# Kernel tuning notes

Measured on AMD Instinct MI355X. Metric: run time of the kernel, lower is better.

The kernel has to match this reference:

```python
import jax, jax.numpy as jnp
import numpy as np

N_NODES = 50000
N_EDGES = 400000
NUM_FEAT = 11
HID = 64
LAT = 64
HEADS = 3
MAX_NODES = 29
NUM_GRAPHS = 2048
NEG_SLOPE = 0.2


def _w(key, shape):
    return (jax.random.normal(key, shape) * 0.05).astype(jnp.float32)


def setup_inputs() -> dict:
    key = jax.random.key(0)
    ks = jax.random.split(key, 32)
    x = jax.random.normal(ks[0], (N_NODES, NUM_FEAT), dtype=jnp.float32)
    edge_index = jax.random.randint(ks[1], (2, N_EDGES), 0, N_NODES, dtype=jnp.int64)
    batch = jnp.sort(jax.random.randint(ks[2], (N_NODES,), 0, NUM_GRAPHS, dtype=jnp.int64))
    d = {"x": x, "edge_index": edge_index, "batch": batch}
    # GATv2 layer params: lin_l, lin_r ([in, heads*out]), att [heads,out], bias [out]
    dims = [(NUM_FEAT, HID), (HID, 2 * HID), (2 * HID, 4 * HID)]
    k = 3
    for i, (cin, cout) in enumerate(dims, start=1):
        d[f"Wl{i}"] = _w(ks[k], (cin, HEADS * cout)); k += 1
        d[f"bl{i}"] = jnp.zeros((HEADS * cout,), jnp.float32)
        d[f"Wr{i}"] = _w(ks[k], (cin, HEADS * cout)); k += 1
        d[f"br{i}"] = jnp.zeros((HEADS * cout,), jnp.float32)
        d[f"att{i}"] = _w(ks[k], (HEADS, cout)); k += 1
        d[f"b{i}"] = jnp.zeros((cout,), jnp.float32)
    d["Wmu"] = _w(ks[k], (4 * HID, LAT)); k += 1
    d["bmu"] = jnp.zeros((LAT,), jnp.float32)
    d["Wlv"] = _w(ks[k], (4 * HID, LAT)); k += 1
    d["blv"] = jnp.zeros((LAT,), jnp.float32)
    out_dim = MAX_NODES * NUM_FEAT + MAX_NODES * MAX_NODES
    d["Wd1"] = _w(ks[k], (LAT, 4 * HID)); k += 1
    d["bd1"] = jnp.zeros((4 * HID,), jnp.float32)
    d["Wd2"] = _w(ks[k], (4 * HID, 8 * HID)); k += 1
    d["bd2"] = jnp.zeros((8 * HID,), jnp.float32)
    d["Wd3"] = _w(ks[k], (8 * HID, out_dim)); k += 1
    d["bd3"] = jnp.zeros((out_dim,), jnp.float32)
    return d


def _gatv2(x, src, dst, Wl, bl, Wr, br, att, bias):
    # GATv2Conv, heads=HEADS, concat=False (mean over heads), self-loops already in src/dst
    N = x.shape[0]
    H, C = att.shape
    xl = (x @ Wl + bl).reshape(N, H, C)  # source transform
    xr = (x @ Wr + br).reshape(N, H, C)  # target transform
    e = jax.nn.leaky_relu(xl[src] + xr[dst], NEG_SLOPE)  # [E,H,C]
    logits = jnp.einsum('ehc,hc->eh', e, att)            # [E,H]
    mx = jax.ops.segment_max(logits, dst, num_segments=N)
    a = jnp.exp(logits - mx[dst])
    denom = jax.ops.segment_sum(a, dst, num_segments=N)
    alpha = a / (denom[dst] + 1e-16)
    out = jax.ops.segment_sum(alpha[:, :, None] * xl[src], dst, num_segments=N)  # [N,H,C]
    return out.mean(axis=1) + bias


def reference(x, edge_index, batch,
              Wl1, bl1, Wr1, br1, att1, b1,
              Wl2, bl2, Wr2, br2, att2, b2,
              Wl3, bl3, Wr3, br3, att3, b3,
              Wmu, bmu, Wlv, blv,
              Wd1, bd1, Wd2, bd2, Wd3, bd3):
    N = x.shape[0]
    loops = jnp.arange(N, dtype=edge_index.dtype)
    src = jnp.concatenate([edge_index[0], loops])
    dst = jnp.concatenate([edge_index[1], loops])
    h = jax.nn.relu(_gatv2(x, src, dst, Wl1, bl1, Wr1, br1, att1, b1))
    h = jax.nn.relu(_gatv2(h, src, dst, Wl2, bl2, Wr2, br2, att2, b2))
    h = jax.nn.relu(_gatv2(h, src, dst, Wl3, bl3, Wr3, br3, att3, b3))
    g = jax.ops.segment_sum(h, batch, num_segments=NUM_GRAPHS)  # global_add_pool
    mu = g @ Wmu + bmu
    logvar = g @ Wlv + blv
    z = mu  # deterministic decode of the posterior mean (no forward() given)
    o = jax.nn.relu(z @ Wd1 + bd1)
    o = jax.nn.relu(o @ Wd2 + bd2)
    o = o @ Wd3 + bd3
    nsplit = MAX_NODES * NUM_FEAT
    x_rec = o[:, :nsplit].reshape(-1, MAX_NODES, NUM_FEAT)
    adj = o[:, nsplit:].reshape(-1, MAX_NODES, MAX_NODES)
    adj_rec = (adj + jnp.swapaxes(adj, 1, 2)) / 2
    return (x_rec, adj_rec, mu, logvar)
```

## Files before the change

### kernel.cpp

```cpp
#include <hip/hip_runtime.h>
#include <hip/hip_bf16.h>

typedef __hip_bfloat16 bf16;
typedef unsigned short ushortT;
typedef ushortT u16x2 __attribute__((ext_vector_type(2)));
typedef ushortT u16x4 __attribute__((ext_vector_type(4)));
typedef ushortT u16x8 __attribute__((ext_vector_type(8)));
typedef __bf16   bf16x8 __attribute__((ext_vector_type(8)));
typedef float    f32x4  __attribute__((ext_vector_type(4)));

#define N_NODES    50000
#define E_EDGES    400000
#define E_TOT      450000
#define NUM_GRAPHS 2048
#define SCAN_CHUNK 1024
#define N_CHUNKS   ((N_NODES + SCAN_CHUNK - 1) / SCAN_CHUNK)

__device__ __forceinline__ float fromb(ushortT u) {
    unsigned int i = ((unsigned int)u) << 16;
    return __builtin_bit_cast(float, i);
}
__device__ __forceinline__ ushortT tob(float v) {
    bf16 h = __float2bfloat16(v);
    return __builtin_bit_cast(ushortT, h);
}

template <int VEC> struct RawV;
template <> struct RawV<1> { using T = ushortT; };
template <> struct RawV<2> { using T = u16x2; };
template <> struct RawV<4> { using T = u16x4; };

__device__ __forceinline__ void cvtv(ushortT r, float* f) { f[0] = fromb(r); }
__device__ __forceinline__ void cvtv(u16x2 r, float* f)   { f[0] = fromb(r.x); f[1] = fromb(r.y); }
__device__ __forceinline__ void cvtv(u16x4 r, float* f)   { f[0] = fromb(r.x); f[1] = fromb(r.y);
                                                            f[2] = fromb(r.z); f[3] = fromb(r.w); }

__global__ void diag_kernel(float* out, float v) { if (threadIdx.x == 0) out[0] = v; }

__global__ void hist_kernel(const int* __restrict__ ei, int* __restrict__ counts) {
    int e = blockIdx.x * 256 + threadIdx.x;
    if (e >= E_TOT) return;
    int d = (e < E_EDGES) ? ei[E_EDGES + e] : (e - E_EDGES);
    atomicAdd(&counts[d], 1);
}

__global__ __launch_bounds__(256) void scan_sums(const int* __restrict__ counts,
                                                 int* __restrict__ chunk_sums) {
    __shared__ int red[4];
    int base = blockIdx.x * SCAN_CHUNK;
    int t = threadIdx.x;
    int s = 0;
    #pragma unroll
    for (int i = 0; i < 4; i++) {
        int idx = base + t + i * 256;
        if (idx < N_NODES) s += counts[idx];
    }
    #pragma unroll
    for (int o = 32; o > 0; o >>= 1) s += __shfl_xor(s, o);
    if ((t & 63) == 0) red[t >> 6] = s;
    __syncthreads();
    if (t == 0) chunk_sums[blockIdx.x] = red[0] + red[1] + red[2] + red[3];
}

__global__ __launch_bounds__(64) void scan_chunks(const int* __restrict__ chunk_sums,
                                                  int* __restrict__ chunk_base) {
    int t = threadIdx.x;
    int v = (t < N_CHUNKS) ? chunk_sums[t] : 0;
    int orig = v;
    #pragma unroll
    for (int o = 1; o < 64; o <<= 1) {
        int u = __shfl_up(v, o);
        if (t >= o) v += u;
    }
    if (t < N_CHUNKS) chunk_base[t] = v - orig;
}

__global__ __launch_bounds__(256) void scan_write(const int* __restrict__ counts,
                                                  const int* __restrict__ chunk_base,
                                                  int* __restrict__ offsets) {
    __shared__ int wsum[4];
    int chunk = blockIdx.x;
    int base = chunk * SCAN_CHUNK;
    int t = threadIdx.x;
    int lane = t & 63, w = t >> 6;

    int c[4];
    int e0 = base + t * 4;
    #pragma unroll
    for (int k = 0; k < 4; k++) {
        int idx = e0 + k;
        c[k] = (idx < N_NODES) ? counts[idx] : 0;
    }
    int local = c[0] + c[1] + c[2] + c[3];

    int v = local;
    #pragma unroll
    for (int o = 1; o < 64; o <<= 1) {
        int u = __shfl_up(v, o);
        if (lane >= o) v += u;
    }
    if (lane == 63) wsum[w] = v;
    __syncthreads();
    int wbase = 0;
    for (int i = 0; i < w; i++) wbase += wsum[i];

    int run = chunk_base[chunk] + wbase + (v - local);
    #pragma unroll
    for (int k = 0; k < 4; k++) {
        int idx = e0 + k;
        if (idx < N_NODES) offsets[idx] = run;
        run += c[k];
    }
    if (chunk == 0 && t == 0) offsets[N_NODES] = E_TOT;
}

__global__ void copy_kernel(const int* __restrict__ src, int* __restrict__ dst, int n) {
    int i = blockIdx.x * 256 + threadIdx.x;
    if (i < n) dst[i] = src[i];
}

__global__ void scatter_kernel(const int* __restrict__ ei, int* __restrict__ cursor,
                               int* __restrict__ srcs) {
    int e = blockIdx.x * 256 + threadIdx.x;
    if (e >= E_TOT) return;
    int s, d;
    if (e < E_EDGES) { s = ei[e]; d = ei[E_EDGES + e]; }
    else             { s = d = e - E_EDGES; }
    int pos = atomicAdd(&cursor[d], 1);
    srcs[pos] = s;
}

__global__ void repack_kernel(const float* __restrict__ W, ushortT* __restrict__ Bp,
                              int K, int N) {
    int idx = blockIdx.x * 256 + threadIdx.x;
    if (idx >= K * N) return;
    int k = idx / N, n = idx % N;
    Bp[((size_t)(k >> 3) * N + n) * 8 + (k & 7)] = tob(W[idx]);
}

__global__ void repack_split(const float* __restrict__ W, ushortT* __restrict__ Bh,
                             ushortT* __restrict__ Bl, int K, int N, int Npad) {
    int idx = blockIdx.x * 256 + threadIdx.x;
    if (idx >= K * Npad) return;
    int k = idx / Npad, n = idx % Npad;
    float v = (n < N) ? W[(size_t)k * N + n] : 0.f;
    ushortT h = tob(v);
    float r = v - fromb(h);
    size_t o = ((size_t)(k >> 3) * Npad + n) * 8 + (k & 7);
    Bh[o] = h;
    Bl[o] = tob(r);
}

__global__ __launch_bounds__(192) void l1_transform(const float* __restrict__ x,
                                                    const float* __restrict__ Wl,
                                                    const float* __restrict__ bl,
                                                    const float* __restrict__ Wr,
                                                    const float* __restrict__ br,
                                                    ushortT* __restrict__ XL,
                                                    ushortT* __restrict__ XR, int M) {
    __shared__ float xs[64][11];
    const int tid = threadIdx.x;
    const int bm  = blockIdx.x * 64;
    const int rows = (M - bm < 64) ? (M - bm) : 64;

    float wl[11], wr[11];
    #pragma unroll
    for (int k = 0; k < 11; k++) {
        wl[k] = Wl[k * 192 + tid];
        wr[k] = Wr[k * 192 + tid];
    }
    float blc = bl[tid], brc = br[tid];

    for (int i = tid; i < rows * 11; i += 192)
        xs[i / 11][i % 11] = x[(size_t)bm * 11 + i];
    __syncthreads();

    for (int r = 0; r < rows; r++) {
        float al = blc, ar = brc;
        #pragma unroll
        for (int k = 0; k < 11; k++) {
            float xv = xs[r][k];
            al += xv * wl[k];
            ar += xv * wr[k];
        }
        size_t o = (size_t)(bm + r) * 192 + tid;
        XL[o] = tob(al);
        XR[o] = tob(ar);
    }
}

template <bool RELU>
__global__ __launch_bounds__(256) void gemm_dec(const float* __restrict__ A,
                                                const float* __restrict__ B,
                                                const float* __restrict__ bias,
                                                float* __restrict__ C,
                                                int M, int N, int K,
                                                int lda, int ldb, int ldc) {
    __shared__ float As[32][33];
    __shared__ float Bs[32][65];
    int tid = threadIdx.x;
    int tm = tid >> 4, tn = tid & 15;
    int bm = blockIdx.y * 32, bn = blockIdx.x * 64;
    float acc[2][4] = {};
    for (int k0 = 0; k0 < K; k0 += 32) {
        #pragma unroll
        for (int i = 0; i < 4; i++) {
            int e = tid + i * 256;
            int r = e >> 5, k = e & 31;
            int row = bm + r, kk = k0 + k;
            float v = 0.f;
            if (row < M && kk < K) v = A[(size_t)row * lda + kk];
            As[k][r] = v;
        }
        #pragma unroll
        for (int i = 0; i < 8; i++) {
            int e = tid + i * 256;
            int k = e >> 6, n = e & 63;
            int kk = k0 + k, col = bn + n;
            float v = 0.f;
            if (kk < K && col < N) v = B[(size_t)kk * ldb + col];
            Bs[k][n] = v;
        }
        __syncthreads();
        #pragma unroll
        for (int k = 0; k < 32; k++) {
            float a0 = As[k][tm * 2 + 0], a1 = As[k][tm * 2 + 1];
            float b0 = Bs[k][tn * 4 + 0], b1 = Bs[k][tn * 4 + 1];
            float b2 = Bs[k][tn * 4 + 2], b3 = Bs[k][tn * 4 + 3];
            acc[0][0] += a0 * b0; acc[0][1] += a0 * b1; acc[0][2] += a0 * b2; acc[0][3] += a0 * b3;
            acc[1][0] += a1 * b0; acc[1][1] += a1 * b1; acc[1][2] += a1 * b2; acc[1][3] += a1 * b3;
        }
        __syncthreads();
    }
    #pragma unroll
    for (int i = 0; i < 2; i++) {
        int row = bm + tm * 2 + i;
        if (row >= M) continue;
        #pragma unroll
        for (int j = 0; j < 4; j++) {
            int col = bn + tn * 4 + j;
            if (col >= N) continue;
            float v = acc[i][j] + bias[col];
            if (RELU) v = fmaxf(v, 0.f);
            C[(size_t)row * ldc + col] = v;
        }
    }
}

template <bool RELU>
__global__ __launch_bounds__(256) void mfma_dec(const float* __restrict__ A,
                                                const ushortT* __restrict__ Bh,
                                                const ushortT* __restrict__ Bl,
                                                const float* __restrict__ bias,
                                                float* __restrict__ C,
                                                int M, int N, int K, int Npad,
                                                int lda, int ldc) {
    __shared__ ushortT Ah[4 * 128 * 8];
    __shared__ ushortT Al[4 * 128 * 8];
    const int tid = threadIdx.x;
    const int bm = blockIdx.y * 128;
    const int bn = blockIdx.x * 128;
    const int lane = tid & 63;
    const int l15 = lane & 15, lg = lane >> 4;
    const int wid = tid >> 6;
    const int wm = wid >> 1, wn = wid & 1;

    f32x4 acc[4][4] = {};

    for (int k0 = 0; k0 < K; k0 += 32) {
        __syncthreads();
        #pragma unroll
        for (int it = 0; it < 2; it++) {
            int c = tid + it * 256;
            int row = c >> 2, kg = c & 3;
            const float* ap = A + (size_t)(bm + row) * lda + k0 + kg * 8;
            u16x8 hv, lv;
            #pragma unroll
            for (int i = 0; i < 8; i++) {
                float v = ap[i];
                ushortT h = tob(v);
                hv[i] = h;
                lv[i] = tob(v - fromb(h));
            }
            int unit = (kg * 128 + row) ^ kg;
            *reinterpret_cast<u16x8*>(&Ah[unit * 8]) = hv;
            *reinterpret_cast<u16x8*>(&Al[unit * 8]) = lv;
        }
        __syncthreads();

        bf16x8 ah[4], al[4], bhf[4], blf[4];
        #pragma unroll
        for (int mf = 0; mf < 4; mf++) {
            int row = wm * 64 + mf * 16 + l15;
            int unit = (lg * 128 + row) ^ lg;
            ah[mf] = __builtin_bit_cast(bf16x8, *reinterpret_cast<const u16x8*>(&Ah[unit * 8]));
            al[mf] = __builtin_bit_cast(bf16x8, *reinterpret_cast<const u16x8*>(&Al[unit * 8]));
        }
        int kgG = (k0 >> 3) + lg;
        #pragma unroll
        for (int nf = 0; nf < 4; nf++) {
            int n = bn + wn * 64 + nf * 16 + l15;
            size_t o = ((size_t)kgG * Npad + n) * 8;
            bhf[nf] = __builtin_bit_cast(bf16x8, *reinterpret_cast<const u16x8*>(Bh + o));
            blf[nf] = __builtin_bit_cast(bf16x8, *reinterpret_cast<const u16x8*>(Bl + o));
        }
        #pragma unroll
        for (int mf = 0; mf < 4; mf++) {
            #pragma unroll
            for (int nf = 0; nf < 4; nf++) {
                acc[mf][nf] = __builtin_amdgcn_mfma_f32_16x16x32_bf16(ah[mf], bhf[nf], acc[mf][nf], 0, 0, 0);
                acc[mf][nf] = __builtin_amdgcn_mfma_f32_16x16x32_bf16(ah[mf], blf[nf], acc[mf][nf], 0, 0, 0);
                acc[mf][nf] = __builtin_amdgcn_mfma_f32_16x16x32_bf16(al[mf], bhf[nf], acc[mf][nf], 0, 0, 0);
            }
        }
    }

    #pragma unroll
    for (int nf = 0; nf < 4; nf++) {
        int col = bn + wn * 64 + nf * 16 + l15;
        if (col >= N) continue;
        float bv = bias[col];
        #pragma unroll
        for (int mf = 0; mf < 4; mf++) {
            #pragma unroll
            for (int q = 0; q < 4; q++) {
                int row = bm + wm * 64 + mf * 16 + lg * 4 + q;
                if (row < M) {
                    float v = acc[mf][nf][q] + bv;
                    if (RELU) v = fmaxf(v, 0.f);
                    C[(size_t)row * ldc + col] = v;
                }
            }
        }
    }
}

template <int K, int CHH>
__global__ __launch_bounds__(256) void mfma_gemm(const ushortT* __restrict__ A,
                                                 const ushortT* __restrict__ BpL,
                                                 const ushortT* __restrict__ BpR,
                                                 const float* __restrict__ bl,
                                                 const float* __restrict__ br,
                                                 bf16* __restrict__ XL,
                                                 bf16* __restrict__ XR,
                                                 int M, int Nfull, int n0) {
    constexpr int KU = K / 8;
    __shared__ ushortT Alds[KU * 128 * 8];
    const int tid = threadIdx.x;
    const int bm  = blockIdx.y * 128;
    const int bnb = blockIdx.x * 128;

    for (int u = tid; u < 128 * KU; u += 256) {
        int row = u / KU, kg = u % KU;
        int rg = bm + row; if (rg > M - 1) rg = M - 1;
        u16x8 v = *reinterpret_cast<const u16x8*>(A + (size_t)rg * K + kg * 8);
        int unit = (kg * 128 + row) ^ (kg & 7);
        *reinterpret_cast<u16x8*>(&Alds[unit * 8]) = v;
    }
    __syncthreads();

    const int lane = tid & 63;
    const int l15 = lane & 15, lg = lane >> 4;
    const int wid = tid >> 6;
    const int wm = wid >> 1, wn = wid & 1;

    f32x4 acc[4][4] = {};
    #pragma unroll
    for (int s = 0; s < K / 32; s++) {
        int kg = s * 4 + lg;
        bf16x8 a[4], b[4];
        #pragma unroll
        for (int mf = 0; mf < 4; mf++) {
            int row = wm * 64 + mf * 16 + l15;
            int unit = (kg * 128 + row) ^ (kg & 7);
            a[mf] = __builtin_bit_cast(bf16x8,
                    *reinterpret_cast<const u16x8*>(&Alds[unit * 8]));
        }
        #pragma unroll
        for (int nf = 0; nf < 4; nf++) {
            int cb = bnb + wn * 64 + nf * 16;
            const ushortT* bp; int n;
            if (cb < CHH) { bp = BpL; n = n0 + cb + l15; }
            else          { bp = BpR; n = n0 + cb - CHH + l15; }
            b[nf] = __builtin_bit_cast(bf16x8,
                    *reinterpret_cast<const u16x8*>(bp + ((size_t)kg * Nfull + n) * 8));
        }
        #pragma unroll
        for (int mf = 0; mf < 4; mf++)
            #pragma unroll
            for (int nf = 0; nf < 4; nf++)
                acc[mf][nf] = __builtin_amdgcn_mfma_f32_16x16x32_bf16(
                    a[mf], b[nf], acc[mf][nf], 0, 0, 0);
    }

    #pragma unroll
    for (int nf = 0; nf < 4; nf++) {
        int cb = bnb + wn * 64 + nf * 16;
        bf16* Cp; const float* bs; int c;
        if (cb < CHH) { Cp = XL; bs = bl; c = cb + l15; }
        else          { Cp = XR; bs = br; c = cb - CHH + l15; }
        float bv = bs[c];
        #pragma unroll
        for (int mf = 0; mf < 4; mf++) {
            #pragma unroll
            for (int q = 0; q < 4; q++) {
                int r = bm + wm * 64 + mf * 16 + lg * 4 + q;
                if (r < M) Cp[(size_t)r * CHH + c] = __float2bfloat16(acc[mf][nf][q] + bv);
            }
        }
    }
}

template <int CHH, int MODE>
__global__ __launch_bounds__(256) void gat_head(const ushortT* __restrict__ XL,
                                                const ushortT* __restrict__ XR,
                                                int ldx, int offx,
                                                const float* __restrict__ att_h,
                                                const float* __restrict__ bias,
                                                const int* __restrict__ offsets,
                                                const int* __restrict__ srcs,
                                                ushortT* __restrict__ OUT, int N) {
    constexpr int VEC = CHH / 64;
    using RT = typename RawV<VEC>::T;
    int wid  = threadIdx.x >> 6;
    int lane = threadIdx.x & 63;
    int n = blockIdx.x * 4 + wid;
    if (n >= N) return;

    float xr_[VEC], a06[VEC], a04[VEC], acc[VEC];
    const ushortT* xrp = XR + (size_t)n * ldx + offx + VEC * lane;
    #pragma unroll
    for (int i = 0; i < VEC; i++) {
        xr_[i] = fromb(xrp[i]);
        float a = att_h[VEC * lane + i];
        a06[i] = 0.6f * a;
        a04[i] = 0.4f * a;
        acc[i] = 0.f;
    }
    float denom = 0.f;

    const int e0 = offsets[n], e1 = offsets[n + 1];
    const int deg = e1 - e0;
    const int loff = offx + VEC * lane;

    for (int base = 0; base < deg; base += 64) {
        int cnt = deg - base; if (cnt > 64) cnt = 64;
        int sl = srcs[e0 + base + ((lane < cnt) ? lane : (cnt - 1))];

        RT pf0, pf1, pf2, pf3;
        pf0 = *reinterpret_cast<const RT*>(XL + (size_t)__shfl(sl, 0) * ldx + loff);
        pf1 = (cnt > 1) ? *reinterpret_cast<const RT*>(XL + (size_t)__shfl(sl, 1) * ldx + loff) : pf0;
        pf2 = (cnt > 2) ? *reinterpret_cast<const RT*>(XL + (size_t)__shfl(sl, 2) * ldx + loff) : pf0;
        pf3 = (cnt > 3) ? *reinterpret_cast<const RT*>(XL + (size_t)__shfl(sl, 3) * ldx + loff) : pf0;

        for (int j = 0; j < cnt; ++j) {
            RT cur = pf0;
            pf0 = pf1; pf1 = pf2; pf2 = pf3;
            if (j + 4 < cnt)
                pf3 = *reinterpret_cast<const RT*>(XL + (size_t)__shfl(sl, j + 4) * ldx + loff);

            float xl[VEC];
            cvtv(cur, xl);
            float part = 0.f;
            #pragma unroll
            for (int i = 0; i < VEC; i++) {
                float v = xl[i] + xr_[i];
                float av = fabsf(v);
                part = fmaf(a06[i], v, part);
                part = fmaf(a04[i], av, part);
            }
            #pragma unroll
            for (int ofs = 32; ofs > 0; ofs >>= 1)
                part += __shfl_xor(part, ofs);

            float w = __expf(part);
            denom += w;
            #pragma unroll
            for (int i = 0; i < VEC; i++) acc[i] = fmaf(w, xl[i], acc[i]);
        }
    }

    float inv = 1.f / (denom + 1e-16f);
    #pragma unroll
    for (int i = 0; i < VEC; i++) {
        int c = VEC * lane + i;
        size_t idx = (size_t)n * CHH + c;
        float v = acc[i] * inv;
        if (MODE > 0) v += fromb(OUT[idx]);
        if (MODE == 2) { v = v * (1.f / 3.f) + bias[c]; v = fmaxf(v, 0.f); }
        OUT[idx] = tob(v);
    }
}

__global__ void pool_kernel(const ushortT* __restrict__ h3, const int* __restrict__ batch,
                            float* __restrict__ G) {
    int g = blockIdx.x;
    int c = threadIdx.x;
    int lo = 0, hi = N_NODES;
    while (lo < hi) { int mid = (lo + hi) >> 1; if (batch[mid] < g) lo = mid + 1; else hi = mid; }
    int s0 = lo;
    hi = N_NODES;
    while (lo < hi) { int mid = (lo + hi) >> 1; if (batch[mid] < g + 1) lo = mid + 1; else hi = mid; }
    int s1 = lo;
    float sum = 0.f;
    for (int n = s0; n < s1; n++) sum += fromb(h3[(size_t)n * 256 + c]);
    G[(size_t)g * 256 + c] = sum;
}

__global__ void assemble_kernel(const float* __restrict__ o3, float* __restrict__ out) {
    int g = blockIdx.x;
    const float* row = o3 + (size_t)g * 1160;
    float* xrec = out + (size_t)g * 319;
    for (int p = threadIdx.x; p < 319; p += 256) xrec[p] = row[p];
    float* adj = out + 653312 + (size_t)g * 841;
    for (int p = threadIdx.x; p < 841; p += 256) {
        int i = p / 29, j = p % 29;
        adj[p] = 0.5f * (row[319 + p] + row[319 + j * 29 + i]);
    }
}

extern "C" void kernel_launch(void* const* d_in, const int* in_sizes, int n_in,
                              void* d_out, int out_size, void* d_ws, size_t ws_size,
                              hipStream_t stream) {
    const float* x     = (const float*)d_in[0];
    const int*   ei    = (const int*)d_in[1];
    const int*   batch = (const int*)d_in[2];
    const float* Wl1 = (const float*)d_in[3];
    const float* bl1 = (const float*)d_in[4];
    const float* Wr1 = (const float*)d_in[5];
    const float* br1 = (const float*)d_in[6];
    const float* att1= (const float*)d_in[7];
    const float* b1  = (const float*)d_in[8];
    const float* Wl2 = (const float*)d_in[9];
    const float* bl2 = (const float*)d_in[10];
    const float* Wr2 = (const float*)d_in[11];
    const float* br2 = (const float*)d_in[12];
    const float* att2= (const float*)d_in[13];
    const float* b2  = (const float*)d_in[14];
    const float* Wl3 = (const float*)d_in[15];
    const float* bl3 = (const float*)d_in[16];
    const float* Wr3 = (const float*)d_in[17];
    const float* br3 = (const float*)d_in[18];
    const float* att3= (const float*)d_in[19];
    const float* b3  = (const float*)d_in[20];
    const float* Wmu = (const float*)d_in[21];
    const float* bmu = (const float*)d_in[22];
    const float* Wlv = (const float*)d_in[23];
    const float* blv = (const float*)d_in[24];
    const float* Wd1 = (const float*)d_in[25];
    const float* bd1 = (const float*)d_in[26];
    const float* Wd2 = (const float*)d_in[27];
    const float* bd2 = (const float*)d_in[28];
    const float* Wd3 = (const float*)d_in[29];
    const float* bd3 = (const float*)d_in[30];
    float* out = (float*)d_out;

    char* wsb = (char*)d_ws;
    ushortT* h3u = (ushortT*)(wsb + 0);
    ushortT* h1u = (ushortT*)(wsb + 0);
    ushortT* h2u = (ushortT*)(wsb + 25600000);
    bf16*    XLb = (bf16*)(wsb + 38400000);
    ushortT* XLu = (ushortT*)(wsb + 38400000);
    bf16*    XRb = (bf16*)(wsb + 64000000);
    ushortT* XRu = (ushortT*)(wsb + 64000000);
    float* G  = (float*)(wsb + 38400000);
    float* O1 = G  + 524288;
    float* O2 = O1 + 524288;
    float* O3 = O2 + 1048576;
    ushortT* BhD3 = (ushortT*)(wsb + 64000000);
    ushortT* BlD3 = (ushortT*)(wsb + 65400000);
    ushortT* BhD2 = (ushortT*)(wsb + 66800000);
    ushortT* BlD2 = (ushortT*)(wsb + 67100000);
    ushortT* BhD1 = (ushortT*)(wsb + 67400000);
    ushortT* BlD1 = (ushortT*)(wsb + 67500000);
    int* counts  = (int*)(wsb + 89600000);
    int* offsets = counts + (N_NODES + 1);
    int* cursor  = offsets + (N_NODES + 1);
    int* srcs    = cursor + (N_NODES + 1);
    int* chunk_sums = srcs + E_TOT;
    int* chunk_base = chunk_sums + 64;
    ushortT* BpL2 = (ushortT*)(wsb + 92000528);
    ushortT* BpR2 = (ushortT*)(wsb + 92049680);
    ushortT* BpL3 = (ushortT*)(wsb + 92098832);
    ushortT* BpR3 = (ushortT*)(wsb + 92295440);

    size_t needed = 92492048;
    if (ws_size < needed) {
        hipLaunchKernelGGL(diag_kernel, dim3(1), dim3(64), 0, stream, out, (float)(ws_size >> 20));
        return;
    }

    const int MU_OFF = 2375680;
    const int LV_OFF = 2506752;

    hipMemsetAsync(counts, 0, sizeof(int) * (N_NODES + 1), stream);
    hipLaunchKernelGGL(hist_kernel, dim3((E_TOT + 255) / 256), dim3(256), 0, stream, ei, counts);
    hipLaunchKernelGGL(scan_sums,   dim3(N_CHUNKS), dim3(256), 0, stream, counts, chunk_sums);
    hipLaunchKernelGGL(scan_chunks, dim3(1), dim3(64), 0, stream, chunk_sums, chunk_base);
    hipLaunchKernelGGL(scan_write,  dim3(N_CHUNKS), dim3(256), 0, stream,
                       counts, chunk_base, offsets);
    hipLaunchKernelGGL(copy_kernel, dim3((N_NODES + 255) / 256), dim3(256), 0, stream,
                       offsets, cursor, N_NODES);
    hipLaunchKernelGGL(scatter_kernel, dim3((E_TOT + 255) / 256), dim3(256), 0, stream,
                       ei, cursor, srcs);

    hipLaunchKernelGGL(repack_kernel, dim3((64 * 384 + 255) / 256), dim3(256), 0, stream,
                       Wl2, BpL2, 64, 384);
    hipLaunchKernelGGL(repack_kernel, dim3((64 * 384 + 255) / 256), dim3(256), 0, stream,
                       Wr2, BpR2, 64, 384);
    hipLaunchKernelGGL(repack_kernel, dim3((128 * 768 + 255) / 256), dim3(256), 0, stream,
                       Wl3, BpL3, 128, 768);
    hipLaunchKernelGGL(repack_kernel, dim3((128 * 768 + 255) / 256), dim3(256), 0, stream,
                       Wr3, BpR3, 128, 768);

    const dim3 AGG_GRID(N_NODES / 4);

    hipLaunchKernelGGL(l1_transform, dim3((N_NODES + 63) / 64), dim3(192), 0, stream,
                       x, Wl1, bl1, Wr1, br1, XLu, XRu, N_NODES);
    hipLaunchKernelGGL((gat_head<64, 0>), AGG_GRID, dim3(256), 0, stream,
                       XLu, XRu, 192, 0,   att1 + 0,   b1, offsets, srcs, h1u, N_NODES);
    hipLaunchKernelGGL((gat_head<64, 1>), AGG_GRID, dim3(256), 0, stream,
                       XLu, XRu, 192, 64,  att1 + 64,  b1, offsets, srcs, h1u, N_NODES);
    hipLaunchKernelGGL((gat_head<64, 2>), AGG_GRID, dim3(256), 0, stream,
                       XLu, XRu, 192, 128, att1 + 128, b1, offsets, srcs, h1u, N_NODES);

    for (int h = 0; h < 3; ++h) {
        hipLaunchKernelGGL((mfma_gemm<64, 128>), dim3(2, 391), dim3(256), 0, stream,
                           h1u, BpL2, BpR2, bl2 + h * 128, br2 + h * 128,
                           XLb, XRb, N_NODES, 384, h * 128);
        if (h == 0)      hipLaunchKernelGGL((gat_head<128, 0>), AGG_GRID, dim3(256), 0, stream,
                             XLu, XRu, 128, 0, att2 + h * 128, b2, offsets, srcs, h2u, N_NODES);
        else if (h == 1) hipLaunchKernelGGL((gat_head<128, 1>), AGG_GRID, dim3(256), 0, stream,
                             XLu, XRu, 128, 0, att2 + h * 128, b2, offsets, srcs, h2u, N_NODES);
        else             hipLaunchKernelGGL((gat_head<128, 2>), AGG_GRID, dim3(256), 0, stream,
                             XLu, XRu, 128, 0, att2 + h * 128, b2, offsets, srcs, h2u, N_NODES);
    }

    for (int h = 0; h < 3; ++h) {
        hipLaunchKernelGGL((mfma_gemm<128, 256>), dim3(4, 391), dim3(256), 0, stream,
                           h2u, BpL3, BpR3, bl3 + h * 256, br3 + h * 256,
                           XLb, XRb, N_NODES, 768, h * 256);
        if (h == 0)      hipLaunchKernelGGL((gat_head<256, 0>), AGG_GRID, dim3(256), 0, stream,
                             XLu, XRu, 256, 0, att3 + h * 256, b3, offsets, srcs, h3u, N_NODES);
        else if (h == 1) hipLaunchKernelGGL((gat_head<256, 1>), AGG_GRID, dim3(256), 0, stream,
                             XLu, XRu, 256, 0, att3 + h * 256, b3, offsets, srcs, h3u, N_NODES);
        else             hipLaunchKernelGGL((gat_head<256, 2>), AGG_GRID, dim3(256), 0, stream,
                             XLu, XRu, 256, 0, att3 + h * 256, b3, offsets, srcs, h3u, N_NODES);
    }

    hipLaunchKernelGGL(repack_split, dim3((64 * 256 + 255) / 256), dim3(256), 0, stream,
                       Wd1, BhD1, BlD1, 64, 256, 256);
    hipLaunchKernelGGL(repack_split, dim3((256 * 512 + 255) / 256), dim3(256), 0, stream,
                       Wd2, BhD2, BlD2, 256, 512, 512);
    hipLaunchKernelGGL(repack_split, dim3((512 * 1280 + 255) / 256), dim3(256), 0, stream,
                       Wd3, BhD3, BlD3, 512, 1160, 1280);

    hipLaunchKernelGGL(pool_kernel, dim3(NUM_GRAPHS), dim3(256), 0, stream, h3u, batch, G);

    hipLaunchKernelGGL((gemm_dec<false>), dim3(1, 64), dim3(256), 0, stream,
                       G, Wmu, bmu, out + MU_OFF, NUM_GRAPHS, 64, 256, 256, 64, 64);
    hipLaunchKernelGGL((gemm_dec<false>), dim3(1, 64), dim3(256), 0, stream,
                       G, Wlv, blv, out + LV_OFF, NUM_GRAPHS, 64, 256, 256, 64, 64);
    hipLaunchKernelGGL((mfma_dec<true>), dim3(2, 16), dim3(256), 0, stream,
                       out + MU_OFF, BhD1, BlD1, bd1, O1, NUM_GRAPHS, 256, 64, 256, 64, 256);
    hipLaunchKernelGGL((mfma_dec<true>), dim3(4, 16), dim3(256), 0, stream,
                       O1, BhD2, BlD2, bd2, O2, NUM_GRAPHS, 512, 256, 512, 256, 512);
    hipLaunchKernelGGL((mfma_dec<false>), dim3(10, 16), dim3(256), 0, stream,
                       O2, BhD3, BlD3, bd3, O3, NUM_GRAPHS, 1160, 512, 1280, 512, 1160);
    hipLaunchKernelGGL(assemble_kernel, dim3(NUM_GRAPHS), dim3(256), 0, stream, O3, out);
}
```

Before: 992.6 us.

## Fuse all three attention heads into one aggregation pass with full-width transforms

When the workspace is large enough, each GATv2 layer's transform is computed for all three heads in a single GEMM launch instead of one per head. Aggregation then uses one kernel that handles all heads together, replacing three per-head passes. This walks each node's edge list and its source indices once rather than three times, and drops the read-modify-write of the partial output between heads. In exchange it needs roughly twice the workspace for the full-width XL/XR buffers and more registers per thread, which may lower occupancy for the 256-channel layer. The old per-head path is kept as a fallback when the workspace is smaller.

```diff
diff --git a/kernel.cpp b/kernel.cpp
--- a/kernel.cpp
+++ b/kernel.cpp
@@ -411,6 +411,82 @@
     }
 }
 
+template <int K, int NW>
+__global__ __launch_bounds__(256) void mfma_gemmF(const ushortT* __restrict__ A,
+                                                  const ushortT* __restrict__ BpL,
+                                                  const ushortT* __restrict__ BpR,
+                                                  const float* __restrict__ bl,
+                                                  const float* __restrict__ br,
+                                                  bf16* __restrict__ XL,
+                                                  bf16* __restrict__ XR,
+                                                  int M) {
+    constexpr int KU = K / 8;
+    __shared__ ushortT Alds[KU * 128 * 8];
+    const int tid = threadIdx.x;
+    const int bm  = blockIdx.y * 128;
+    const int bnb = blockIdx.x * 128;
+
+    for (int u = tid; u < 128 * KU; u += 256) {
+        int row = u / KU, kg = u % KU;
+        int rg = bm + row; if (rg > M - 1) rg = M - 1;
+        u16x8 v = *reinterpret_cast<const u16x8*>(A + (size_t)rg * K + kg * 8);
+        int unit = (kg * 128 + row) ^ (kg & 7);
+        *reinterpret_cast<u16x8*>(&Alds[unit * 8]) = v;
+    }
+    __syncthreads();
+
+    const int lane = tid & 63;
+    const int l15 = lane & 15, lg = lane >> 4;
+    const int wid = tid >> 6;
+    const int wm = wid >> 1, wn = wid & 1;
+
+    f32x4 acc[4][4] = {};
+    #pragma unroll
+    for (int s = 0; s < K / 32; s++) {
+        int kg = s * 4 + lg;
+        bf16x8 a[4], b[4];
+        #pragma unroll
+        for (int mf = 0; mf < 4; mf++) {
+            int row = wm * 64 + mf * 16 + l15;
+            int unit = (kg * 128 + row) ^ (kg & 7);
+            a[mf] = __builtin_bit_cast(bf16x8,
+                    *reinterpret_cast<const u16x8*>(&Alds[unit * 8]));
+        }
+        #pragma unroll
+        for (int nf = 0; nf < 4; nf++) {
+            int cb = bnb + wn * 64 + nf * 16;
+            const ushortT* bp; int n;
+            if (cb < NW) { bp = BpL; n = cb + l15; }
+            else         { bp = BpR; n = cb - NW + l15; }
+            b[nf] = __builtin_bit_cast(bf16x8,
+                    *reinterpret_cast<const u16x8*>(bp + ((size_t)kg * NW + n) * 8));
+        }
+        #pragma unroll
+        for (int mf = 0; mf < 4; mf++)
+            #pragma unroll
+            for (int nf = 0; nf < 4; nf++)
+                acc[mf][nf] = __builtin_amdgcn_mfma_f32_16x16x32_bf16(
+                    a[mf], b[nf], acc[mf][nf], 0, 0, 0);
+    }
+
+    #pragma unroll
+    for (int nf = 0; nf < 4; nf++) {
+        int cb = bnb + wn * 64 + nf * 16;
+        bf16* Cp; const float* bs; int c;
+        if (cb < NW) { Cp = XL; bs = bl; c = cb + l15; }
+        else         { Cp = XR; bs = br; c = cb - NW + l15; }
+        float bv = bs[c];
+        #pragma unroll
+        for (int mf = 0; mf < 4; mf++) {
+            #pragma unroll
+            for (int q = 0; q < 4; q++) {
+                int r = bm + wm * 64 + mf * 16 + lg * 4 + q;
+                if (r < M) Cp[(size_t)r * NW + c] = __float2bfloat16(acc[mf][nf][q] + bv);
+            }
+        }
+    }
+}
+
 template <int CHH, int MODE>
 __global__ __launch_bounds__(256) void gat_head(const ushortT* __restrict__ XL,
                                                 const ushortT* __restrict__ XR,
@@ -489,6 +565,111 @@
         if (MODE > 0) v += fromb(OUT[idx]);
         if (MODE == 2) { v = v * (1.f / 3.f) + bias[c]; v = fmaxf(v, 0.f); }
         OUT[idx] = tob(v);
+    }
+}
+
+template <int CHH>
+__global__ __launch_bounds__(256) void gat_fused(const ushortT* __restrict__ XL,
+                                                 const ushortT* __restrict__ XR,
+                                                 const float* __restrict__ att,
+                                                 const float* __restrict__ bias,
+                                                 const int* __restrict__ offsets,
+                                                 const int* __restrict__ srcs,
+                                                 ushortT* __restrict__ OUT, int N) {
+    constexpr int VEC = CHH / 64;
+    constexpr int LDX = 3 * CHH;
+    using RT = typename RawV<VEC>::T;
+    int wid  = threadIdx.x >> 6;
+    int lane = threadIdx.x & 63;
+    int n = blockIdx.x * 4 + wid;
+    if (n >= N) return;
+
+    float xr_[3][VEC], a06[3][VEC], a04[3][VEC], acc[3][VEC];
+    const ushortT* xrp = XR + (size_t)n * LDX + VEC * lane;
+    #pragma unroll
+    for (int h = 0; h < 3; h++) {
+        #pragma unroll
+        for (int i = 0; i < VEC; i++) {
+            xr_[h][i] = fromb(xrp[h * CHH + i]);
+            float a = att[h * CHH + VEC * lane + i];
+            a06[h][i] = 0.6f * a;
+            a04[h][i] = 0.4f * a;
+            acc[h][i] = 0.f;
+        }
+    }
+    float d0 = 0.f, d1 = 0.f, d2 = 0.f;
+
+    const int e0 = offsets[n], e1 = offsets[n + 1];
+    const int deg = e1 - e0;
+    const int loff = VEC * lane;
+
+    for (int base = 0; base < deg; base += 64) {
+        int cnt = deg - base; if (cnt > 64) cnt = 64;
+        int sl = srcs[e0 + base + ((lane < cnt) ? lane : (cnt - 1))];
+
+        RT pA0, pA1, pA2, pB0, pB1, pB2;
+        {
+            const ushortT* r = XL + (size_t)__shfl(sl, 0) * LDX + loff;
+            pA0 = *reinterpret_cast<const RT*>(r);
+            pA1 = *reinterpret_cast<const RT*>(r + CHH);
+            pA2 = *reinterpret_cast<const RT*>(r + 2 * CHH);
+        }
+        if (cnt > 1) {
+            const ushortT* r = XL + (size_t)__shfl(sl, 1) * LDX + loff;
+            pB0 = *reinterpret_cast<const RT*>(r);
+            pB1 = *reinterpret_cast<const RT*>(r + CHH);
+            pB2 = *reinterpret_cast<const RT*>(r + 2 * CHH);
+        } else { pB0 = pA0; pB1 = pA1; pB2 = pA2; }
+
+        for (int j = 0; j < cnt; ++j) {
+            RT c0 = pA0, c1 = pA1, c2 = pA2;
+            pA0 = pB0; pA1 = pB1; pA2 = pB2;
+            if (j + 2 < cnt) {
+                const ushortT* r = XL + (size_t)__shfl(sl, j + 2) * LDX + loff;
+                pB0 = *reinterpret_cast<const RT*>(r);
+                pB1 = *reinterpret_cast<const RT*>(r + CHH);
+                pB2 = *reinterpret_cast<const RT*>(r + 2 * CHH);
+            }
+
+            float xl0[VEC], xl1[VEC], xl2[VEC];
+            cvtv(c0, xl0); cvtv(c1, xl1); cvtv(c2, xl2);
+            float p0 = 0.f, p1 = 0.f, p2 = 0.f;
+            #pragma unroll
+            for (int i = 0; i < VEC; i++) {
+                float v0 = xl0[i] + xr_[0][i];
+                float v1 = xl1[i] + xr_[1][i];
+                float v2 = xl2[i] + xr_[2][i];
+                p0 = fmaf(a06[0][i], v0, p0); p0 = fmaf(a04[0][i], fabsf(v0), p0);
+                p1 = fmaf(a06[1][i], v1, p1); p1 = fmaf(a04[1][i], fabsf(v1), p1);
+                p2 = fmaf(a06[2][i], v2, p2); p2 = fmaf(a04[2][i], fabsf(v2), p2);
+            }
+            #pragma unroll
+            for (int ofs = 32; ofs > 0; ofs >>= 1) {
+                p0 += __shfl_xor(p0, ofs);
+                p1 += __shfl_xor(p1, ofs);
+                p2 += __shfl_xor(p2, ofs);
+            }
+
+            float w0 = __expf(p0), w1 = __expf(p1), w2 = __expf(p2);
+            d0 += w0; d1 += w1; d2 += w2;
+            #pragma unroll
+            for (int i = 0; i < VEC; i++) {
+                acc[0][i] = fmaf(w0, xl0[i], acc[0][i]);
+                acc[1][i] = fmaf(w1, xl1[i], acc[1][i]);
+                acc[2][i] = fmaf(w2, xl2[i], acc[2][i]);
+            }
+        }
+    }
+
+    float i0 = 1.f / (d0 + 1e-16f);
+    float i1 = 1.f / (d1 + 1e-16f);
+    float i2 = 1.f / (d2 + 1e-16f);
+    #pragma unroll
+    for (int i = 0; i < VEC; i++) {
+        int c = VEC * lane + i;
+        float v = (acc[0][i] * i0 + acc[1][i] * i1 + acc[2][i] * i2) * (1.f / 3.f) + bias[c];
+        v = fmaxf(v, 0.f);
+        OUT[(size_t)n * CHH + c] = tob(v);
     }
 }
 
@@ -555,7 +736,105 @@
     const float* bd3 = (const float*)d_in[30];
     float* out = (float*)d_out;
 
+    const int MU_OFF = 2375680;
+    const int LV_OFF = 2506752;
     char* wsb = (char*)d_ws;
+
+    const size_t NEED_FULL = 194892064;
+    const size_t NEED_FB   = 92492048;
+
+    const dim3 AGG_GRID(N_NODES / 4);
+
+    if (ws_size >= NEED_FULL) {
+        ushortT* h3u = (ushortT*)(wsb + 0);
+        ushortT* h1u = (ushortT*)(wsb + 0);
+        ushortT* h2u = (ushortT*)(wsb + 25600000);
+        bf16*    XLb = (bf16*)(wsb + 38400000);
+        ushortT* XLu = (ushortT*)(wsb + 38400000);
+        bf16*    XRb = (bf16*)(wsb + 115200000);
+        ushortT* XRu = (ushortT*)(wsb + 115200000);
+        float* G  = (float*)(wsb + 38400000);
+        float* O1 = G  + 524288;
+        float* O2 = O1 + 524288;
+        float* O3 = O2 + 1048576;
+        ushortT* BhD3 = (ushortT*)(wsb + 115200000);
+        ushortT* BlD3 = (ushortT*)(wsb + 116600000);
+        ushortT* BhD2 = (ushortT*)(wsb + 118000000);
+        ushortT* BlD2 = (ushortT*)(wsb + 118300000);
+        ushortT* BhD1 = (ushortT*)(wsb + 118600000);
+        ushortT* BlD1 = (ushortT*)(wsb + 118700000);
+        int* counts  = (int*)(wsb + 192000000);
+        int* offsets = counts + (N_NODES + 1);
+        int* cursor  = offsets + (N_NODES + 1);
+        int* srcs    = cursor + (N_NODES + 1);
+        int* chunk_sums = srcs + E_TOT;
+        int* chunk_base = chunk_sums + 64;
+        ushortT* BpL2 = (ushortT*)(wsb + 194400544);
+        ushortT* BpR2 = (ushortT*)(wsb + 194449696);
+        ushortT* BpL3 = (ushortT*)(wsb + 194498848);
+        ushortT* BpR3 = (ushortT*)(wsb + 194695456);
+
+        hipMemsetAsync(counts, 0, sizeof(int) * (N_NODES + 1), stream);
+        hipLaunchKernelGGL(hist_kernel, dim3((E_TOT + 255) / 256), dim3(256), 0, stream, ei, counts);
+        hipLaunchKernelGGL(scan_sums,   dim3(N_CHUNKS), dim3(256), 0, stream, counts, chunk_sums);
+        hipLaunchKernelGGL(scan_chunks, dim3(1), dim3(64), 0, stream, chunk_sums, chunk_base);
+        hipLaunchKernelGGL(scan_write,  dim3(N_CHUNKS), dim3(256), 0, stream,
+                           counts, chunk_base, offsets);
+        hipLaunchKernelGGL(copy_kernel, dim3((N_NODES + 255) / 256), dim3(256), 0, stream,
+                           offsets, cursor, N_NODES);
+        hipLaunchKernelGGL(scatter_kernel, dim3((E_TOT + 255) / 256), dim3(256), 0, stream,
+                           ei, cursor, srcs);
+
+        hipLaunchKernelGGL(repack_kernel, dim3((64 * 384 + 255) / 256), dim3(256), 0, stream,
+                           Wl2, BpL2, 64, 384);
+        hipLaunchKernelGGL(repack_kernel, dim3((64 * 384 + 255) / 256), dim3(256), 0, stream,
+                           Wr2, BpR2, 64, 384);
+        hipLaunchKernelGGL(repack_kernel, dim3((128 * 768 + 255) / 256), dim3(256), 0, stream,
+                           Wl3, BpL3, 128, 768);
+        hipLaunchKernelGGL(repack_kernel, dim3((128 * 768 + 255) / 256), dim3(256), 0, stream,
+                           Wr3, BpR3, 128, 768);
+
+        hipLaunchKernelGGL(l1_transform, dim3((N_NODES + 63) / 64), dim3(192), 0, stream,
+                           x, Wl1, bl1, Wr1, br1, XLu, XRu, N_NODES);
+        hipLaunchKernelGGL((gat_fused<64>), AGG_GRID, dim3(256), 0, stream,
+                           XLu, XRu, att1, b1, offsets, srcs, h1u, N_NODES);
+        hipLaunchKernelGGL((mfma_gemmF<64, 384>), dim3(6, 391), dim3(256), 0, stream,
+                           h1u, BpL2, BpR2, bl2, br2, XLb, XRb, N_NODES);
+        hipLaunchKernelGGL((gat_fused<128>), AGG_GRID, dim3(256), 0, stream,
+                           XLu, XRu, att2, b2, offsets, srcs, h2u, N_NODES);
+        hipLaunchKernelGGL((mfma_gemmF<128, 768>), dim3(12, 391), dim3(256), 0, stream,
+                           h2u, BpL3, BpR3, bl3, br3, XLb, XRb, N_NODES);
+        hipLaunchKernelGGL((gat_fused<256>), AGG_GRID, dim3(256), 0, stream,
+                           XLu, XRu, att3, b3, offsets, srcs, h3u, N_NODES);
+
+        hipLaunchKernelGGL(repack_split, dim3((64 * 256 + 255) / 256), dim3(256), 0, stream,
+                           Wd1, BhD1, BlD1, 64, 256, 256);
+        hipLaunchKernelGGL(repack_split, dim3((256 * 512 + 255) / 256), dim3(256), 0, stream,
+                           Wd2, BhD2, BlD2, 256, 512, 512);
+        hipLaunchKernelGGL(repack_split, dim3((512 * 1280 + 255) / 256), dim3(256), 0, stream,
+                           Wd3, BhD3, BlD3, 512, 1160, 1280);
+
+        hipLaunchKernelGGL(pool_kernel, dim3(NUM_GRAPHS), dim3(256), 0, stream, h3u, batch, G);
+
+        hipLaunchKernelGGL((gemm_dec<false>), dim3(1, 64), dim3(256), 0, stream,
+                           G, Wmu, bmu, out + MU_OFF, NUM_GRAPHS, 64, 256, 256, 64, 64);
+        hipLaunchKernelGGL((gemm_dec<false>), dim3(1, 64), dim3(256), 0, stream,
+                           G, Wlv, blv, out + LV_OFF, NUM_GRAPHS, 64, 256, 256, 64, 64);
+        hipLaunchKernelGGL((mfma_dec<true>), dim3(2, 16), dim3(256), 0, stream,
+                           out + MU_OFF, BhD1, BlD1, bd1, O1, NUM_GRAPHS, 256, 64, 256, 64, 256);
+        hipLaunchKernelGGL((mfma_dec<true>), dim3(4, 16), dim3(256), 0, stream,
+                           O1, BhD2, BlD2, bd2, O2, NUM_GRAPHS, 512, 256, 512, 256, 512);
+        hipLaunchKernelGGL((mfma_dec<false>), dim3(10, 16), dim3(256), 0, stream,
+                           O2, BhD3, BlD3, bd3, O3, NUM_GRAPHS, 1160, 512, 1280, 512, 1160);
+        hipLaunchKernelGGL(assemble_kernel, dim3(NUM_GRAPHS), dim3(256), 0, stream, O3, out);
+        return;
+    }
+
+    if (ws_size < NEED_FB) {
+        hipLaunchKernelGGL(diag_kernel, dim3(1), dim3(64), 0, stream, out, (float)(ws_size >> 20));
+        return;
+    }
+
     ushortT* h3u = (ushortT*)(wsb + 0);
     ushortT* h1u = (ushortT*)(wsb + 0);
     ushortT* h2u = (ushortT*)(wsb + 25600000);
@@ -584,15 +863,6 @@
     ushortT* BpL3 = (ushortT*)(wsb + 92098832);
     ushortT* BpR3 = (ushortT*)(wsb + 92295440);
 
-    size_t needed = 92492048;
-    if (ws_size < needed) {
-        hipLaunchKernelGGL(diag_kernel, dim3(1), dim3(64), 0, stream, out, (float)(ws_size >> 20));
-        return;
-    }
-
-    const int MU_OFF = 2375680;
-    const int LV_OFF = 2506752;
-
     hipMemsetAsync(counts, 0, sizeof(int) * (N_NODES + 1), stream);
     hipLaunchKernelGGL(hist_kernel, dim3((E_TOT + 255) / 256), dim3(256), 0, stream, ei, counts);
     hipLaunchKernelGGL(scan_sums,   dim3(N_CHUNKS), dim3(256), 0, stream, counts, chunk_sums);
@@ -612,8 +882,6 @@
                        Wl3, BpL3, 128, 768);
     hipLaunchKernelGGL(repack_kernel, dim3((128 * 768 + 255) / 256), dim3(256), 0, stream,
                        Wr3, BpR3, 128, 768);
-
-    const dim3 AGG_GRID(N_NODES / 4);
 
     hipLaunchKernelGGL(l1_transform, dim3((N_NODES + 63) / 64), dim3(192), 0, stream,
                        x, Wl1, bl1, Wr1, br1, XLu, XRu, N_NODES);
```

After: 846.3 us. -14.7%, faster.
